# Kernel tuning notes

Hardware: AMD Instinct MI355X
Metric: run time of the kernel (lower is better)

The kernel has to match this reference:

```python
import jax, jax.numpy as jnp
import numpy as np

CUTOFF = 5.0
NLINKED = 1
CELL_LIST = CUTOFF / NLINKED  # linked-cell edge length
_r = np.arange(-NLINKED, NLINKED + 1)
# torch.cartesian_prod(r1,r1,r1) == meshgrid(indexing='ij') stacked & flattened
LINKED = np.stack(np.meshgrid(_r, _r, _r, indexing='ij'), axis=-1).reshape(1, -1, 3).astype(np.float32)  # (1, 27, 3)


def setup_inputs() -> dict:
    N = 2744
    L = 30.0
    key = jax.random.key(0)
    k1, k2 = jax.random.split(key)
    coordinates = jax.random.uniform(k1, (N, 3), dtype=jnp.float32) * L
    cell = jnp.eye(3, dtype=jnp.float32) * L
    mass = jax.random.uniform(k2, (N,), dtype=jnp.float32) * 15.0 + 1.0
    period_table = jnp.ones((3,), dtype=jnp.int32)  # fully periodic
    return {"period_table": period_table, "coordinates": coordinates, "cell": cell, "mass": mass}


def _forward(period_table, coordinates, cell, mass):
    numatom = coordinates.shape[0]
    # wrap coordinates into the cell relative to atom 0 (fractional coords)
    inv_cell = jnp.linalg.inv(cell)
    inv_coor = coordinates @ inv_cell
    inv_coor = inv_coor - jnp.round(inv_coor - inv_coor[0])
    coordinates = inv_coor @ cell
    # remove center of mass
    com = (mass @ coordinates) / jnp.sum(mass)
    coordinates = coordinates - com[None, :]
    # periodic replicas needed to cover the cutoff
    num_repeats = jnp.ceil(jnp.min(CUTOFF / jnp.abs(cell), axis=0)).astype(jnp.int32)
    num_repeats = period_table.astype(jnp.int32) * num_repeats
    up = num_repeats + 1
    down = -num_repeats
    rs = [jnp.arange(int(down[i]), int(up[i])) for i in range(3)]
    g = jnp.meshgrid(*rs, indexing='ij')
    shifts_frac = jnp.stack(g, axis=-1).reshape(-1, 3).astype(coordinates.dtype)  # (S, 3)
    shifts = shifts_frac @ cell  # (S, 3) cartesian shift vectors
    num_shifts = shifts.shape[0]
    # prod = cartesian_prod(all_shifts, all_atoms).T : row0 shift idx, row1 atom idx
    prod0 = jnp.repeat(jnp.arange(num_shifts), numatom)
    prod1 = jnp.tile(jnp.arange(numatom), num_shifts)
    # shift box so all coords are positive; pad by cutoff
    mincoor = jnp.min(coordinates, axis=0) - CUTOFF - 1e-6
    coordinates = coordinates - mincoor
    maxcoor = jnp.max(coordinates, axis=0) + CUTOFF
    # all periodic images, keep only those inside the padded box
    image = (coordinates[None, :, :] + shifts[:, None, :]).reshape(-1, 3)
    keep = jnp.nonzero(((image < maxcoor) & (image > 0)).all(axis=1))[0]
    image_mask = image[keep]                      # (M, 3)
    prod0 = prod0[keep]
    prod1 = prod1[keep]
    # linked-cell indices
    ori_image_index = jnp.floor(coordinates / CELL_LIST)         # (N, 3)
    neigh_cell = ori_image_index[:, None, :] + jnp.asarray(LINKED)  # (N, 27, 3)
    image_index = jnp.floor(image_mask / CELL_LIST)              # (M, 3)
    max_cell_index = jnp.ceil(maxcoor / CELL_LIST)
    f10 = max_cell_index[1] * max_cell_index[0]
    neigh_cell_index = neigh_cell[:, :, 2] * f10 + neigh_cell[:, :, 1] * max_cell_index[0] + neigh_cell[:, :, 0]  # (N, 27)
    nimage_index = image_index[:, 2] * f10 + image_index[:, 1] * max_cell_index[0] + image_index[:, 0]            # (M,)
    # dense (N, M, 27) cell-index equality -- the memory-bound hot spot
    eq = neigh_cell_index[:, None, :] == nimage_index[None, :, None]
    ai, aj, _ = jnp.nonzero(eq)
    # distance filter on candidate pairs
    d = jnp.linalg.norm(coordinates[ai] - image_mask[aj], axis=-1)
    pair = jnp.nonzero((d < CUTOFF) & (d > 0.001))[0]
    center = ai[pair]
    img = aj[pair]
    shift_idx = prod0[img]
    atom_j = prod1[img]
    neigh_list = jnp.stack([center, atom_j])  # (2, P)
    return neigh_list, shifts[shift_idx], shifts_frac, shift_idx


def reference(period_table, coordinates, cell, mass):
    neigh_list, shifts_out, _, _ = _forward(period_table, coordinates, cell, mass)
    return (neigh_list, shifts_out)
```

## Files before the change

kernel.cpp:

```cpp
#include <hip/hip_runtime.h>
#include <math.h>

#define S_CAP   27
#define MAXNB   128
#define CAPQ    128
#define CUT     5.0f
#define NTHR    256
#define NTHC    512
#define GRP     64
#define NMAX    2744


__device__ __forceinline__ void load_cell(const float* __restrict__ cell, float c[3][3])
{
    #pragma unroll
    for (int i = 0; i < 3; i++)
        #pragma unroll
        for (int j = 0; j < 3; j++) c[i][j] = cell[3 * i + j];
}

__device__ __forceinline__ void header_and_shifts(
    const float c[3][3], const int* __restrict__ period,
    const double* __restrict__ pd, const float* __restrict__ pf, int nblkA,
    float* sF, int* sI, float* s_shifts)
{
    #pragma clang fp contract(off)
    int t = threadIdx.x;
    if (t < 64) {
        double SM = 0.0, SX = 0.0, SY = 0.0, SZ = 0.0;
        float MN0 =  __builtin_inff(), MN1 =  __builtin_inff(), MN2 =  __builtin_inff();
        float MX0 = -__builtin_inff(), MX1 = -__builtin_inff(), MX2 = -__builtin_inff();
        for (int b = t; b < nblkA; b += 64) {
            SM += pd[4*b+0]; SX += pd[4*b+1]; SY += pd[4*b+2]; SZ += pd[4*b+3];
            MN0 = fminf(MN0, pf[6*b+0]); MN1 = fminf(MN1, pf[6*b+1]); MN2 = fminf(MN2, pf[6*b+2]);
            MX0 = fmaxf(MX0, pf[6*b+3]); MX1 = fmaxf(MX1, pf[6*b+4]); MX2 = fmaxf(MX2, pf[6*b+5]);
        }
        #pragma unroll
        for (int off = 32; off > 0; off >>= 1) {
            SM += __shfl_down(SM, off, 64);
            SX += __shfl_down(SX, off, 64);
            SY += __shfl_down(SY, off, 64);
            SZ += __shfl_down(SZ, off, 64);
            MN0 = fminf(MN0, __shfl_down(MN0, off, 64));
            MN1 = fminf(MN1, __shfl_down(MN1, off, 64));
            MN2 = fminf(MN2, __shfl_down(MN2, off, 64));
            MX0 = fmaxf(MX0, __shfl_down(MX0, off, 64));
            MX1 = fmaxf(MX1, __shfl_down(MX1, off, 64));
            MX2 = fmaxf(MX2, __shfl_down(MX2, off, 64));
        }
        if (t == 0) {
            float den  = (float)SM;
            float com0 = ((float)SX) / den;
            float com1 = ((float)SY) / den;
            float com2 = ((float)SZ) / den;
            float m20 = ((MN0 - com0) - CUT) - 1e-6f;
            float m21 = ((MN1 - com1) - CUT) - 1e-6f;
            float m22 = ((MN2 - com2) - CUT) - 1e-6f;
            float maxc0 = ((MX0 - com0) - m20) + CUT;
            float maxc1 = ((MX1 - com1) - m21) + CUT;
            float maxc2 = ((MX2 - com2) - m22) + CUT;
            float mcell0 = ceilf(maxc0 / CUT);
            float mcell1 = ceilf(maxc1 / CUT);
            float f10 = mcell1 * mcell0;
            int nr[3];
            for (int j = 0; j < 3; j++) {
                float v = __builtin_inff();
                for (int i = 0; i < 3; i++) {
                    float q = CUT / fabsf(c[i][j]);
                    v = fminf(v, q);
                }
                nr[j] = (int)ceilf(v);
                nr[j] *= period[j];
            }
            int nsz0 = 2*nr[0]+1, nsz1 = 2*nr[1]+1, nsz2 = 2*nr[2]+1;
            int S = nsz0 * nsz1 * nsz2;
            if (S > S_CAP) S = S_CAP;
            sI[0] = S;
            sI[1] = -nr[0]; sI[2] = -nr[1]; sI[3] = -nr[2];
            sI[4] = nsz1;   sI[5] = nsz2;
            sF[0] = maxc0; sF[1] = maxc1; sF[2] = maxc2;
            sF[3] = f10;   sF[4] = mcell0;
            sF[5] = m20;   sF[6] = m21;   sF[7] = m22;
            sF[8] = com0;  sF[9] = com1;  sF[10] = com2;
        }
    }
    __syncthreads();
    int S = sI[0];
    if (t < S) {
        int n1 = sI[4], n2 = sI[5];
        int i0 = t / (n1 * n2);
        int rem = t - i0 * n1 * n2;
        int i1 = rem / n2;
        int i2 = rem - i1 * n2;
        float fx = (float)(sI[1] + i0);
        float fy = (float)(sI[2] + i1);
        float fz = (float)(sI[3] + i2);
        #pragma unroll
        for (int d = 0; d < 3; d++)
            s_shifts[3*t + d] = fx*c[0][d] + fy*c[1][d] + fz*c[2][d];
    }
    __syncthreads();
}

__global__ __launch_bounds__(NTHR)
void kA_wrap(const float* __restrict__ coor, const float* __restrict__ cell,
             const float* __restrict__ mass, float* __restrict__ xv,
             int* __restrict__ sc_agg,
             int* __restrict__ grp_sum, int* __restrict__ grp_arrive,
             double* __restrict__ pd, float* __restrict__ pf, int n, int nagg, int ng)
{
    #pragma clang fp contract(off)
    __shared__ double wsum[4][4];
    __shared__ float  wred[4][6];
    int t    = threadIdx.x;
    int bid  = blockIdx.x;
    int gtid = bid * NTHR + t;
    int lane = t & 63;
    int w    = t >> 6;

    if (gtid < nagg) sc_agg[gtid] = -1;
    if (gtid < ng)   { grp_sum[gtid] = -1; grp_arrive[gtid] = 0; }

    float c[3][3];
    load_cell(cell, c);
    float a00 = c[1][1]*c[2][2] - c[1][2]*c[2][1];
    float a01 = c[0][2]*c[2][1] - c[0][1]*c[2][2];
    float a02 = c[0][1]*c[1][2] - c[0][2]*c[1][1];
    float a10 = c[1][2]*c[2][0] - c[1][0]*c[2][2];
    float a11 = c[0][0]*c[2][2] - c[0][2]*c[2][0];
    float a12 = c[0][2]*c[1][0] - c[0][0]*c[1][2];
    float a20 = c[1][0]*c[2][1] - c[1][1]*c[2][0];
    float a21 = c[0][1]*c[2][0] - c[0][0]*c[2][1];
    float a22 = c[0][0]*c[1][1] - c[0][1]*c[1][0];
    float det = c[0][0]*a00 + c[0][1]*a10 + c[0][2]*a20;
    float inv[3][3] = {{a00/det, a01/det, a02/det},
                       {a10/det, a11/det, a12/det},
                       {a20/det, a21/det, a22/det}};
    float f0[3];
    #pragma unroll
    for (int d = 0; d < 3; d++)
        f0[d] = coor[0]*inv[0][d] + coor[1]*inv[1][d] + coor[2]*inv[2][d];

    double sm = 0.0, sx = 0.0, sy = 0.0, sz = 0.0;
    float mn0 =  __builtin_inff(), mn1 =  __builtin_inff(), mn2 =  __builtin_inff();
    float mx0 = -__builtin_inff(), mx1 = -__builtin_inff(), mx2 = -__builtin_inff();
    if (gtid < n) {
        float p0 = coor[3*gtid], p1 = coor[3*gtid+1], p2 = coor[3*gtid+2];
        float ic[3], ww[3], x[3];
        #pragma unroll
        for (int d = 0; d < 3; d++)
            ic[d] = p0*inv[0][d] + p1*inv[1][d] + p2*inv[2][d];
        #pragma unroll
        for (int d = 0; d < 3; d++)
            ww[d] = ic[d] - rintf(ic[d] - f0[d]);
        #pragma unroll
        for (int d = 0; d < 3; d++)
            x[d] = ww[0]*c[0][d] + ww[1]*c[1][d] + ww[2]*c[2][d];
        xv[3*gtid] = x[0]; xv[3*gtid+1] = x[1]; xv[3*gtid+2] = x[2];
        float m = mass[gtid];
        sm = (double)m;
        sx = (double)m * (double)x[0];
        sy = (double)m * (double)x[1];
        sz = (double)m * (double)x[2];
        mn0 = x[0]; mn1 = x[1]; mn2 = x[2];
        mx0 = x[0]; mx1 = x[1]; mx2 = x[2];
    }
    #pragma unroll
    for (int off = 32; off > 0; off >>= 1) {
        sm += __shfl_down(sm, off, 64);
        sx += __shfl_down(sx, off, 64);
        sy += __shfl_down(sy, off, 64);
        sz += __shfl_down(sz, off, 64);
        mn0 = fminf(mn0, __shfl_down(mn0, off, 64));
        mn1 = fminf(mn1, __shfl_down(mn1, off, 64));
        mn2 = fminf(mn2, __shfl_down(mn2, off, 64));
        mx0 = fmaxf(mx0, __shfl_down(mx0, off, 64));
        mx1 = fmaxf(mx1, __shfl_down(mx1, off, 64));
        mx2 = fmaxf(mx2, __shfl_down(mx2, off, 64));
    }
    if (lane == 0) {
        wsum[w][0] = sm; wsum[w][1] = sx; wsum[w][2] = sy; wsum[w][3] = sz;
        wred[w][0] = mn0; wred[w][1] = mn1; wred[w][2] = mn2;
        wred[w][3] = mx0; wred[w][4] = mx1; wred[w][5] = mx2;
    }
    __syncthreads();
    if (t == 0) {
        double SM = 0.0, SX = 0.0, SY = 0.0, SZ = 0.0;
        float MN0 =  __builtin_inff(), MN1 =  __builtin_inff(), MN2 =  __builtin_inff();
        float MX0 = -__builtin_inff(), MX1 = -__builtin_inff(), MX2 = -__builtin_inff();
        #pragma unroll
        for (int q = 0; q < 4; q++) {
            SM += wsum[q][0]; SX += wsum[q][1]; SY += wsum[q][2]; SZ += wsum[q][3];
            MN0 = fminf(MN0, wred[q][0]); MN1 = fminf(MN1, wred[q][1]); MN2 = fminf(MN2, wred[q][2]);
            MX0 = fmaxf(MX0, wred[q][3]); MX1 = fmaxf(MX1, wred[q][4]); MX2 = fmaxf(MX2, wred[q][5]);
        }
        pd[bid*4+0] = SM; pd[bid*4+1] = SX; pd[bid*4+2] = SY; pd[bid*4+3] = SZ;
        pf[bid*6+0] = MN0; pf[bid*6+1] = MN1; pf[bid*6+2] = MN2;
        pf[bid*6+3] = MX0; pf[bid*6+4] = MX1; pf[bid*6+5] = MX2;
    }
}

__global__ __launch_bounds__(NTHC, 6)
void kC_search_emit(const int* __restrict__ period, const float* __restrict__ cell,
                    const double* __restrict__ pd, const float* __restrict__ pf,
                    const float* __restrict__ xv,
                    int* __restrict__ sc_agg, int* __restrict__ grp_sum,
                    int* __restrict__ grp_arrive,
                    float* __restrict__ out, int nblkA, int nblkC, int n, int P)
{
    #pragma clang fp contract(off)
    __shared__ float sF[12];
    __shared__ int   sI[8];
    __shared__ float s_shifts[3 * S_CAP];
    __shared__ float sux[NMAX], suy[NMAX], suz[NMAX];
    __shared__ int   que[8][CAPQ];
    __shared__ int   lst[8][MAXNB];
    __shared__ int   s_np[8];
    __shared__ int   sExcl;
    __shared__ int   sFin;

    const int t    = threadIdx.x;
    const int bid  = blockIdx.x;
    const int lane = t & 63;
    const int w    = t >> 6;
    const int g    = bid / GRP;
    const int gpos = bid - g * GRP;
    const int gbase = g * GRP;
    const int gsz  = min(GRP, nblkC - gbase);

    if (n > NMAX) return;

    float c[3][3];
    load_cell(cell, c);
    header_and_shifts(c, period, pd, pf, nblkA, sF, sI, s_shifts);

    float a00 = c[1][1]*c[2][2] - c[1][2]*c[2][1];
    float a01 = c[0][2]*c[2][1] - c[0][1]*c[2][2];
    float a02 = c[0][1]*c[1][2] - c[0][2]*c[1][1];
    float a10 = c[1][2]*c[2][0] - c[1][0]*c[2][2];
    float a11 = c[0][0]*c[2][2] - c[0][2]*c[2][0];
    float a12 = c[0][2]*c[1][0] - c[0][0]*c[1][2];
    float a20 = c[1][0]*c[2][1] - c[1][1]*c[2][0];
    float a21 = c[0][1]*c[2][0] - c[0][0]*c[2][1];
    float a22 = c[0][0]*c[1][1] - c[0][1]*c[1][0];
    float det = c[0][0]*a00 + c[0][1]*a10 + c[0][2]*a20;
    float inv[3][3] = {{a00/det, a01/det, a02/det},
                       {a10/det, a11/det, a12/det},
                       {a20/det, a21/det, a22/det}};

    const bool diag = (c[0][1]==0.0f) && (c[0][2]==0.0f) && (c[1][0]==0.0f) &&
                      (c[1][2]==0.0f) && (c[2][0]==0.0f) && (c[2][1]==0.0f);
    const float L0 = c[0][0], L1 = c[1][1], L2 = c[2][2];
    const float iL0 = inv[0][0], iL1 = inv[1][1], iL2 = inv[2][2];
    const float PRETH = CUT*CUT + 0.02f;

    {
        const float m20 = sF[5], m21 = sF[6], m22 = sF[7];
        const float com0 = sF[8], com1 = sF[9], com2 = sF[10];
        for (int j = t; j < n; j += NTHC) {
            sux[j] = (xv[3*j]   - com0) - m20;
            suy[j] = (xv[3*j+1] - com1) - m21;
            suz[j] = (xv[3*j+2] - com2) - m22;
        }
    }
    __syncthreads();

    const int atom = bid * 4 + (w >> 1);
    const int half = w & 1;
    const bool valid = atom < n;

    int cnt = 0;
    if (valid) {
        const float xi = sux[atom], yi = suy[atom], zi = suz[atom];
        const int nh = (n + 1) >> 1;
        const int jlo = half * nh;
        const int jhi = min(n, jlo + nh);

        int qcnt = 0;
        for (int jb = jlo; jb < jhi; jb += 64) {
            int j = jb + lane;
            bool pre = false;
            if (j < jhi) {
                float dx = xi - sux[j], dy = yi - suy[j], dz = zi - suz[j];
                float ssp;
                if (diag) {
                    float f0r = dx - L0 * rintf(dx * iL0);
                    float f1r = dy - L1 * rintf(dy * iL1);
                    float f2r = dz - L2 * rintf(dz * iL2);
                    ssp = f0r*f0r + f1r*f1r + f2r*f2r;
                } else {
                    float fr0 = rintf(dx*inv[0][0] + dy*inv[1][0] + dz*inv[2][0]);
                    float fr1 = rintf(dx*inv[0][1] + dy*inv[1][1] + dz*inv[2][1]);
                    float fr2 = rintf(dx*inv[0][2] + dy*inv[1][2] + dz*inv[2][2]);
                    float ddx = dx - (fr0*c[0][0] + fr1*c[1][0] + fr2*c[2][0]);
                    float ddy = dy - (fr0*c[0][1] + fr1*c[1][1] + fr2*c[2][1]);
                    float ddz = dz - (fr0*c[0][2] + fr1*c[1][2] + fr2*c[2][2]);
                    ssp = ddx*ddx + ddy*ddy + ddz*ddz;
                }
                pre = ssp < PRETH;
            }
            unsigned long long m = __ballot(pre);
            int posn = qcnt + (int)__popcll(m & ((1ull << lane) - 1ull));
            if (pre && posn < CAPQ) que[w][posn] = j;
            qcnt += (int)__popcll(m);
        }
        if (qcnt > CAPQ) qcnt = CAPQ;

        const int d0 = sI[1], d1 = sI[2], d2 = sI[3];
        const int nsz1 = sI[4], nsz2 = sI[5];
        for (int qb = 0; qb < qcnt; qb += 64) {
            int r = qb + lane;
            bool ok = false; int gg = 0;
            if (r < qcnt) {
                int j = que[w][r];
                float ujx = sux[j], ujy = suy[j], ujz = suz[j];
                float dx = xi - ujx, dy = yi - ujy, dz = zi - ujz;
                float fr0 = rintf(dx*inv[0][0] + dy*inv[1][0] + dz*inv[2][0]);
                float fr1 = rintf(dx*inv[0][1] + dy*inv[1][1] + dz*inv[2][1]);
                float fr2 = rintf(dx*inv[0][2] + dy*inv[1][2] + dz*inv[2][2]);
                float sx = fr0*c[0][0] + fr1*c[1][0] + fr2*c[2][0];
                float sy = fr0*c[0][1] + fr1*c[1][1] + fr2*c[2][1];
                float sz = fr0*c[0][2] + fr1*c[1][2] + fr2*c[2][2];
                float imx = ujx + sx, imy = ujy + sy, imz = ujz + sz;
                float ddx = xi - imx, ddy = yi - imy, ddz = zi - imz;
                float ss = ddx*ddx + ddy*ddy + ddz*ddz;
                float dd = sqrtf(ss);
                ok = (dd < CUT) && (dd > 0.001f);
                int i0 = (int)fr0 - d0, i1 = (int)fr1 - d1, i2 = (int)fr2 - d2;
                int idx = (i0 * nsz1 + i1) * nsz2 + i2;
                gg = idx * n + j;
            }
            unsigned long long m = __ballot(ok);
            int posn = cnt + (int)__popcll(m & ((1ull << lane) - 1ull));
            if (ok && posn < MAXNB) lst[w][posn] = gg;
            cnt += (int)__popcll(m);
        }
        if (cnt > MAXNB) cnt = MAXNB;
    }
    if (lane == 0) s_np[w] = cnt;
    __syncthreads();

    if (t == 0) {
        int agg = 0;
        #pragma unroll
        for (int q = 0; q < 8; q++) agg += s_np[q];
        __hip_atomic_store(&sc_agg[bid], agg, __ATOMIC_RELAXED, __HIP_MEMORY_SCOPE_AGENT);
        int r = __hip_atomic_fetch_add(&grp_arrive[g], 1, __ATOMIC_ACQ_REL, __HIP_MEMORY_SCOPE_AGENT);
        sFin = (r == gsz - 1) ? 1 : 0;
    }
    __syncthreads();

    if (sFin && w == 0) {
        int idx = gbase + lane;
        int v = 0;
        if (lane < gsz)
            v = __hip_atomic_load(&sc_agg[idx], __ATOMIC_RELAXED, __HIP_MEMORY_SCOPE_AGENT);
        #pragma unroll
        for (int off = 32; off > 0; off >>= 1)
            v += __shfl_down(v, off, 64);
        if (lane == 0)
            __hip_atomic_store(&grp_sum[g], v, __ATOMIC_RELAXED, __HIP_MEMORY_SCOPE_AGENT);
    }

    if (w == 0) {
        int v1 = 0;
        if (lane < g) {
            v1 = __hip_atomic_load(&grp_sum[lane], __ATOMIC_RELAXED, __HIP_MEMORY_SCOPE_AGENT);
            while (v1 == -1) {
                __builtin_amdgcn_s_sleep(2);
                v1 = __hip_atomic_load(&grp_sum[lane], __ATOMIC_RELAXED, __HIP_MEMORY_SCOPE_AGENT);
            }
        }
        int v2 = 0;
        if (lane < gpos) {
            int idx = gbase + lane;
            v2 = __hip_atomic_load(&sc_agg[idx], __ATOMIC_RELAXED, __HIP_MEMORY_SCOPE_AGENT);
            while (v2 == -1) {
                __builtin_amdgcn_s_sleep(2);
                v2 = __hip_atomic_load(&sc_agg[idx], __ATOMIC_RELAXED, __HIP_MEMORY_SCOPE_AGENT);
            }
        }
        int v = v1 + v2;
        #pragma unroll
        for (int off = 32; off > 0; off >>= 1)
            v += __shfl_down(v, off, 64);
        if (lane == 0) sExcl = v;
    }
    __syncthreads();

    if (valid && cnt > 0) {
        const int wa = w & ~1, wb = wa | 1;
        const int cA = s_np[wa], cB = s_np[wb];
        int base = sExcl;
        for (int q = 0; q < wa; q++) base += s_np[q];
        for (int r = lane; r < cnt; r += 64) {
            int gg = lst[w][r];
            int rank = 0;
            for (int q = 0; q < cA; q++) rank += (lst[wa][q] < gg) ? 1 : 0;
            for (int q = 0; q < cB; q++) rank += (lst[wb][q] < gg) ? 1 : 0;
            int p = base + rank;
            if (p < P) {
                int sidx = gg / n;
                int a = gg - sidx * n;
                out[p]     = (float)atom;
                out[P + p] = (float)a;
                out[2*P + 3*p]     = s_shifts[3*sidx];
                out[2*P + 3*p + 1] = s_shifts[3*sidx + 1];
                out[2*P + 3*p + 2] = s_shifts[3*sidx + 2];
            }
        }
    }
}

extern "C" void kernel_launch(void* const* d_in, const int* in_sizes, int n_in,
                              void* d_out, int out_size, void* d_ws, size_t ws_size,
                              hipStream_t stream)
{
    const int*   period = (const int*)d_in[0];
    const float* coor   = (const float*)d_in[1];
    const float* cell   = (const float*)d_in[2];
    const float* mass   = (const float*)d_in[3];
    float* out = (float*)d_out;

    int n = in_sizes[1] / 3;
    int P = out_size / 5;

    char* wp = (char*)d_ws;
    size_t off = 0;
    auto alloc = [&](size_t bytes) -> void* {
        off = (off + 15) & ~(size_t)15;
        void* pp = (void*)(wp + off); off += bytes; return pp;
    };

    int nblkA = (n + NTHR - 1) / NTHR;
    int nblkC = (n + 3) / 4;
    int ng    = (nblkC + GRP - 1) / GRP;

    float*  xv       = (float*) alloc(3 * (size_t)n * 4);
    double* pd       = (double*)alloc((size_t)nblkA * 4 * 8);
    float*  pf       = (float*) alloc((size_t)nblkA * 6 * 4);
    int*    sc_agg   = (int*)   alloc((size_t)nblkC * 4);
    int*    grp_sum  = (int*)   alloc((size_t)ng * 4);
    int*    grp_arr  = (int*)   alloc((size_t)ng * 4);
    (void)ws_size; (void)n_in;

    hipLaunchKernelGGL(kA_wrap, dim3(nblkA), dim3(NTHR), 0, stream,
                       coor, cell, mass, xv, sc_agg, grp_sum, grp_arr,
                       pd, pf, n, nblkC, ng);
    hipLaunchKernelGGL(kC_search_emit, dim3(nblkC), dim3(NTHC), 0, stream,
                       period, cell, pd, pf, xv,
                       sc_agg, grp_sum, grp_arr, out, nblkA, nblkC, n, P);
}
```

Before: 90.06 us.

## Store wrapped coordinates as SoA and read them from global instead of LDS

The first kernel now writes wrapped coordinates into three separate x/y/z arrays instead of one interleaved array. The search kernel no longer stages every atom into about 33 KB of shared memory per block. It reads coordinates directly from global memory (through cache) and recomputes the COM and min offset on each load. This removes a per-block full-array staging pass plus a barrier and frees LDS, which should allow more resident blocks. In exchange every pairwise inner-loop load now goes to global/L2 instead of LDS, and the n<=NMAX limit is removed.

```diff
diff --git a/kernel.cpp b/kernel.cpp
--- a/kernel.cpp
+++ b/kernel.cpp
@@ -8,7 +8,6 @@
 #define NTHR    256
 #define NTHC    512
 #define GRP     64
-#define NMAX    2744
 
 
 __device__ __forceinline__ void load_cell(const float* __restrict__ cell, float c[3][3])
@@ -104,7 +103,8 @@
 
 __global__ __launch_bounds__(NTHR)
 void kA_wrap(const float* __restrict__ coor, const float* __restrict__ cell,
-             const float* __restrict__ mass, float* __restrict__ xv,
+             const float* __restrict__ mass,
+             float* __restrict__ xvx, float* __restrict__ xvy, float* __restrict__ xvz,
              int* __restrict__ sc_agg,
              int* __restrict__ grp_sum, int* __restrict__ grp_arrive,
              double* __restrict__ pd, float* __restrict__ pf, int n, int nagg, int ng)
@@ -156,7 +156,7 @@
         #pragma unroll
         for (int d = 0; d < 3; d++)
             x[d] = ww[0]*c[0][d] + ww[1]*c[1][d] + ww[2]*c[2][d];
-        xv[3*gtid] = x[0]; xv[3*gtid+1] = x[1]; xv[3*gtid+2] = x[2];
+        xvx[gtid] = x[0]; xvy[gtid] = x[1]; xvz[gtid] = x[2];
         float m = mass[gtid];
         sm = (double)m;
         sx = (double)m * (double)x[0];
@@ -203,7 +203,8 @@
 __global__ __launch_bounds__(NTHC, 6)
 void kC_search_emit(const int* __restrict__ period, const float* __restrict__ cell,
                     const double* __restrict__ pd, const float* __restrict__ pf,
-                    const float* __restrict__ xv,
+                    const float* __restrict__ xvx, const float* __restrict__ xvy,
+                    const float* __restrict__ xvz,
                     int* __restrict__ sc_agg, int* __restrict__ grp_sum,
                     int* __restrict__ grp_arrive,
                     float* __restrict__ out, int nblkA, int nblkC, int n, int P)
@@ -212,7 +213,6 @@
     __shared__ float sF[12];
     __shared__ int   sI[8];
     __shared__ float s_shifts[3 * S_CAP];
-    __shared__ float sux[NMAX], suy[NMAX], suz[NMAX];
     __shared__ int   que[8][CAPQ];
     __shared__ int   lst[8][MAXNB];
     __shared__ int   s_np[8];
@@ -227,8 +227,6 @@
     const int gpos = bid - g * GRP;
     const int gbase = g * GRP;
     const int gsz  = min(GRP, nblkC - gbase);
-
-    if (n > NMAX) return;
 
     float c[3][3];
     load_cell(cell, c);
@@ -254,16 +252,8 @@
     const float iL0 = inv[0][0], iL1 = inv[1][1], iL2 = inv[2][2];
     const float PRETH = CUT*CUT + 0.02f;
 
-    {
-        const float m20 = sF[5], m21 = sF[6], m22 = sF[7];
-        const float com0 = sF[8], com1 = sF[9], com2 = sF[10];
-        for (int j = t; j < n; j += NTHC) {
-            sux[j] = (xv[3*j]   - com0) - m20;
-            suy[j] = (xv[3*j+1] - com1) - m21;
-            suz[j] = (xv[3*j+2] - com2) - m22;
-        }
-    }
-    __syncthreads();
+    const float m20 = sF[5], m21 = sF[6], m22 = sF[7];
+    const float com0 = sF[8], com1 = sF[9], com2 = sF[10];
 
     const int atom = bid * 4 + (w >> 1);
     const int half = w & 1;
@@ -271,7 +261,9 @@
 
     int cnt = 0;
     if (valid) {
-        const float xi = sux[atom], yi = suy[atom], zi = suz[atom];
+        const float xi = (xvx[atom] - com0) - m20;
+        const float yi = (xvy[atom] - com1) - m21;
+        const float zi = (xvz[atom] - com2) - m22;
         const int nh = (n + 1) >> 1;
         const int jlo = half * nh;
         const int jhi = min(n, jlo + nh);
@@ -281,7 +273,10 @@
             int j = jb + lane;
             bool pre = false;
             if (j < jhi) {
-                float dx = xi - sux[j], dy = yi - suy[j], dz = zi - suz[j];
+                float ujx = (xvx[j] - com0) - m20;
+                float ujy = (xvy[j] - com1) - m21;
+                float ujz = (xvz[j] - com2) - m22;
+                float dx = xi - ujx, dy = yi - ujy, dz = zi - ujz;
                 float ssp;
                 if (diag) {
                     float f0r = dx - L0 * rintf(dx * iL0);
@@ -313,7 +308,9 @@
             bool ok = false; int gg = 0;
             if (r < qcnt) {
                 int j = que[w][r];
-                float ujx = sux[j], ujy = suy[j], ujz = suz[j];
+                float ujx = (xvx[j] - com0) - m20;
+                float ujy = (xvy[j] - com1) - m21;
+                float ujz = (xvz[j] - com2) - m22;
                 float dx = xi - ujx, dy = yi - ujy, dz = zi - ujz;
                 float fr0 = rintf(dx*inv[0][0] + dy*inv[1][0] + dz*inv[2][0]);
                 float fr1 = rintf(dx*inv[0][1] + dy*inv[1][1] + dz*inv[2][1]);
@@ -436,7 +433,9 @@
     int nblkC = (n + 3) / 4;
     int ng    = (nblkC + GRP - 1) / GRP;
 
-    float*  xv       = (float*) alloc(3 * (size_t)n * 4);
+    float*  xvx      = (float*) alloc((size_t)n * 4);
+    float*  xvy      = (float*) alloc((size_t)n * 4);
+    float*  xvz      = (float*) alloc((size_t)n * 4);
     double* pd       = (double*)alloc((size_t)nblkA * 4 * 8);
     float*  pf       = (float*) alloc((size_t)nblkA * 6 * 4);
     int*    sc_agg   = (int*)   alloc((size_t)nblkC * 4);
@@ -445,9 +444,9 @@
     (void)ws_size; (void)n_in;
 
     hipLaunchKernelGGL(kA_wrap, dim3(nblkA), dim3(NTHR), 0, stream,
-                       coor, cell, mass, xv, sc_agg, grp_sum, grp_arr,
+                       coor, cell, mass, xvx, xvy, xvz, sc_agg, grp_sum, grp_arr,
                        pd, pf, n, nblkC, ng);
     hipLaunchKernelGGL(kC_search_emit, dim3(nblkC), dim3(NTHC), 0, stream,
-                       period, cell, pd, pf, xv,
+                       period, cell, pd, pf, xvx, xvy, xvz,
                        sc_agg, grp_sum, grp_arr, out, nblkA, nblkC, n, P);
 }
```

After: 96.83 us. +7.5%, slower.
